# Kernel tuning notes

Measured on AMD Instinct MI355X. Metric: run time of the kernel, lower is better.

## Reference

```python
import jax, jax.numpy as jnp
import numpy as np

HEADS, DIM_HEAD, LANDMARKS, PINV_ITERS = 8, 64, 256, 6
DIM, SIZE, N_CLASSES, N_PATCH = 512, 1024, 2, 16384
LN_EPS = 1e-5


def layer_norm(x, g, b):
    mu = x.mean(-1, keepdims=True)
    var = ((x - mu) ** 2).mean(-1, keepdims=True)
    return (x - mu) / jnp.sqrt(var + LN_EPS) * g + b


def moore_penrose_pinv(x, iters):
    # x: [b, h, m, m]; global max over all batch/head entries (matches torch.max)
    abs_x = jnp.abs(x)
    col = abs_x.sum(-1).max()
    row = abs_x.sum(-2).max()
    z = jnp.swapaxes(x, -1, -2) / (col * row)
    I = jnp.eye(x.shape[-1], dtype=x.dtype)
    for _ in range(iters):
        xz = x @ z
        z = 0.25 * z @ (13 * I - xz @ (15 * I - xz @ (7 * I - xz)))
    return z


def nystrom_attention(x, qkv_w, out_w, out_b, res_w):
    b, n, _ = x.shape
    m = LANDMARKS
    pad = (m - n % m) % m
    xp = jnp.pad(x, ((0, 0), (pad, 0), (0, 0)))  # pad at FRONT of sequence
    npad = n + pad
    qkv = xp @ qkv_w  # [b, npad, 3*h*d]
    q, k, v = jnp.split(qkv, 3, axis=-1)
    to_h = lambda t: t.reshape(b, npad, HEADS, DIM_HEAD).transpose(0, 2, 1, 3)
    q, k, v = to_h(q), to_h(k), to_h(v)
    q = q * (DIM_HEAD ** -0.5)
    l = npad // m  # tokens per landmark segment
    q_l = q.reshape(b, HEADS, m, l, DIM_HEAD).sum(3) / l
    k_l = k.reshape(b, HEADS, m, l, DIM_HEAD).sum(3) / l
    sim1 = jnp.einsum('bhid,bhjd->bhij', q, k_l)     # [b,h,npad,m]
    sim2 = jnp.einsum('bhid,bhjd->bhij', q_l, k_l)   # [b,h,m,m]
    sim3 = jnp.einsum('bhid,bhjd->bhij', q_l, k)     # [b,h,m,npad]
    a1 = jax.nn.softmax(sim1, -1)
    a2 = jax.nn.softmax(sim2, -1)
    a3 = jax.nn.softmax(sim3, -1)
    out = (a1 @ moore_penrose_pinv(a2, PINV_ITERS)) @ (a3 @ v)
    # residual depthwise conv over sequence dim, kernel (33,1), groups=heads
    res = jax.lax.conv_general_dilated(
        v, res_w, (1, 1), [(16, 16), (0, 0)],
        dimension_numbers=('NCHW', 'OIHW', 'NCHW'), feature_group_count=HEADS)
    out = out + res
    out = out.transpose(0, 2, 1, 3).reshape(b, npad, HEADS * DIM_HEAD)
    out = out @ out_w + out_b
    return out[:, -n:]


def trans_layer(x, ng, nb, qkv_w, out_w, out_b, res_w):
    return x + nystrom_attention(layer_norm(x, ng, nb), qkv_w, out_w, out_b, res_w)


def ppeg(x, w7, b7, w5, b5, w3, b3, H, W):
    cls_tok, feat = x[:, :1], x[:, 1:]
    B, N, C = feat.shape
    f = feat.transpose(0, 2, 1).reshape(B, C, H, W)
    def dw(w, b, p):
        y = jax.lax.conv_general_dilated(
            f, w, (1, 1), [(p, p), (p, p)],
            dimension_numbers=('NCHW', 'OIHW', 'NCHW'), feature_group_count=C)
        return y + b[None, :, None, None]
    out = dw(w7, b7, 3) + f + dw(w5, b5, 2) + dw(w3, b3, 1)
    out = out.reshape(B, C, H * W).transpose(0, 2, 1)
    return jnp.concatenate([cls_tok, out], axis=1)


def setup_inputs() -> dict:
    key = jax.random.key(0)
    ks = jax.random.split(key, 24)
    rn = lambda k, s, sc=0.02: jax.random.normal(k, s, jnp.float32) * sc
    inner = HEADS * DIM_HEAD  # 512
    return {
        'data': jax.random.normal(ks[0], (1, N_PATCH, SIZE), jnp.float32),
        'fc1_w': rn(ks[1], (SIZE, DIM)), 'fc1_b': jnp.zeros((DIM,), jnp.float32),
        'cls_token': jax.random.normal(ks[2], (1, 1, DIM), jnp.float32),
        'l1_ng': jnp.ones((DIM,), jnp.float32), 'l1_nb': jnp.zeros((DIM,), jnp.float32),
        'l1_qkv': rn(ks[3], (DIM, 3 * inner)),
        'l1_ow': rn(ks[4], (inner, DIM)), 'l1_ob': jnp.zeros((DIM,), jnp.float32),
        'l1_rw': rn(ks[5], (HEADS, 1, 33, 1)),
        'l2_ng': jnp.ones((DIM,), jnp.float32), 'l2_nb': jnp.zeros((DIM,), jnp.float32),
        'l2_qkv': rn(ks[6], (DIM, 3 * inner)),
        'l2_ow': rn(ks[7], (inner, DIM)), 'l2_ob': jnp.zeros((DIM,), jnp.float32),
        'l2_rw': rn(ks[8], (HEADS, 1, 33, 1)),
        'p_w7': rn(ks[9], (DIM, 1, 7, 7)), 'p_b7': jnp.zeros((DIM,), jnp.float32),
        'p_w5': rn(ks[10], (DIM, 1, 5, 5)), 'p_b5': jnp.zeros((DIM,), jnp.float32),
        'p_w3': rn(ks[11], (DIM, 1, 3, 3)), 'p_b3': jnp.zeros((DIM,), jnp.float32),
        'n_g': jnp.ones((DIM,), jnp.float32), 'n_b': jnp.zeros((DIM,), jnp.float32),
        'fc2_w': rn(ks[12], (DIM, N_CLASSES)), 'fc2_b': jnp.zeros((N_CLASSES,), jnp.float32),
    }


def reference(data, fc1_w, fc1_b, cls_token, l1_ng, l1_nb, l1_qkv, l1_ow, l1_ob, l1_rw,
              l2_ng, l2_nb, l2_qkv, l2_ow, l2_ob, l2_rw,
              p_w7, p_b7, p_w5, p_b5, p_w3, p_b3, n_g, n_b, fc2_w, fc2_b):
    h = jax.nn.relu(data @ fc1_w + fc1_b)  # [B, N, 512]
    B, N = h.shape[0], h.shape[1]
    _H = _W = int(np.ceil(np.sqrt(N)))
    add_length = _H * _W - N
    h = jnp.concatenate([h, h[:, :add_length, :]], axis=1)
    cls = jnp.broadcast_to(cls_token, (B, 1, h.shape[2]))
    h = jnp.concatenate([cls, h], axis=1)
    h = trans_layer(h, l1_ng, l1_nb, l1_qkv, l1_ow, l1_ob, l1_rw)
    h = ppeg(h, p_w7, p_b7, p_w5, p_b5, p_w3, p_b3, _H, _W)
    h = trans_layer(h, l2_ng, l2_nb, l2_qkv, l2_ow, l2_ob, l2_rw)
    h = layer_norm(h, n_g, n_b)[:, 0]
    logits = h @ fc2_w + fc2_b
    y_hat = jnp.argmax(logits, axis=1)
    y_prob = jax.nn.softmax(logits, axis=1)
    return (logits, y_prob, y_hat)
```

## Files before the change

kernel.cpp:

```cpp
#include <hip/hip_runtime.h>
#include <hip/hip_bf16.h>


#define NT 16385
#define NP 16640
#define PADR 255
#define DIMF 512
#define QKVW 1536
#define NHEAD 8
#define DH 64
#define NLM 256
#define LSEG 65
#define A3V_TC 20

typedef short bf16x8 __attribute__((ext_vector_type(8)));
typedef short bf16x4 __attribute__((ext_vector_type(4)));
typedef float f32x4 __attribute__((ext_vector_type(4)));

__device__ __forceinline__ void gload_lds16(const void* g, void* l) {
    __builtin_amdgcn_global_load_lds(
        (const __attribute__((address_space(1))) void*)g,
        (__attribute__((address_space(3))) void*)l, 16, 0, 0);
}

__device__ __forceinline__ float2 b2f(const __hip_bfloat16* p) {
    ushort2 u = *(const ushort2*)p;
    float2 r;
    r.x = __uint_as_float((unsigned)u.x << 16);
    r.y = __uint_as_float((unsigned)u.y << 16);
    return r;
}

__device__ __forceinline__ unsigned f2b16(float a, float b) {
    union { unsigned u; __hip_bfloat16 h[2]; } c;
    c.h[0] = __float2bfloat16(a); c.h[1] = __float2bfloat16(b);
    return c.u;
}

__device__ __forceinline__ bf16x4 f4b(float a, float b, float c, float d) {
    union { bf16x4 v; __hip_bfloat16 h[4]; } u;
    u.h[0] = __float2bfloat16(a); u.h[1] = __float2bfloat16(b);
    u.h[2] = __float2bfloat16(c); u.h[3] = __float2bfloat16(d);
    return u.v;
}

__global__ __launch_bounds__(256) void gemm_bf16_k(
    const __hip_bfloat16* __restrict__ A, const __hip_bfloat16* __restrict__ BT,
    const float* __restrict__ bias, const float* __restrict__ Cacc,
    float* __restrict__ C, __hip_bfloat16* __restrict__ C16,
    int M, int N, int K, int MA, int relu)
{
    __shared__ __align__(16) __hip_bfloat16 Asl[2][128 * 64];
    __shared__ __align__(16) __hip_bfloat16 Bsl[2][128 * 64];
    int tid = threadIdx.x;
    int wid = tid >> 6, lane = tid & 63;
    int nwg = (int)(gridDim.x * gridDim.y);
    int orig = (int)(blockIdx.y * gridDim.x + blockIdx.x);
    int qq = nwg >> 3, rr = nwg & 7;
    int xcd = orig & 7, idx = orig >> 3;
    int wg = (xcd < rr ? xcd * (qq + 1) : rr * (qq + 1) + (xcd - rr) * qq) + idx;
    int m0 = (wg / (int)gridDim.x) << 7, n0 = (wg % (int)gridDim.x) << 7;
    int wr = (wid >> 1) << 6, wc = (wid & 1) << 6;
    f32x4 acc[4][4] = {};
    int lr = lane >> 3, lk = (lane & 7) << 3;
    int nt = K >> 6;
    auto stage = [&](int buf, int kt) {
#pragma unroll
        for (int i = 0; i < 4; ++i) {
            int ch = wid * 4 + i;
            int rowA = m0 + ch * 8 + lr;
            rowA = rowA < MA ? rowA : (MA - 1);
            gload_lds16(A + (size_t)rowA * K + kt + lk, &Asl[buf][ch * 512]);
            int rowB = n0 + ch * 8 + lr;
            gload_lds16(BT + (size_t)rowB * K + kt + lk, &Bsl[buf][ch * 512]);
        }
    };
    stage(0, 0);
    __syncthreads();
    int cur = 0;
    for (int t = 0; t < nt; ++t) {
        if (t + 1 < nt) stage(cur ^ 1, (t + 1) << 6);
#pragma unroll
        for (int ks = 0; ks < 2; ++ks) {
            int kb = ks * 32 + (lane >> 4) * 8;
            bf16x8 af[4], bfr[4];
#pragma unroll
            for (int m = 0; m < 4; ++m)
                af[m] = *(const bf16x8*)&Asl[cur][(wr + m * 16 + (lane & 15)) * 64 + kb];
#pragma unroll
            for (int n = 0; n < 4; ++n)
                bfr[n] = *(const bf16x8*)&Bsl[cur][(wc + n * 16 + (lane & 15)) * 64 + kb];
#pragma unroll
            for (int m = 0; m < 4; ++m)
#pragma unroll
                for (int n = 0; n < 4; ++n)
                    acc[m][n] = __builtin_amdgcn_mfma_f32_16x16x32_bf16(
                        af[m], bfr[n], acc[m][n], 0, 0, 0);
        }
        __syncthreads();
        cur ^= 1;
    }
    int cr = (lane >> 4) << 2, cc = lane & 15;
#pragma unroll
    for (int m = 0; m < 4; ++m) {
#pragma unroll
        for (int i = 0; i < 4; ++i) {
            int gm = m0 + wr + m * 16 + cr + i;
            if (gm >= M) continue;
#pragma unroll
            for (int n = 0; n < 4; ++n) {
                int gn = n0 + wc + n * 16 + cc;
                float v = acc[m][n][i];
                if (bias) v += bias[gn];
                if (Cacc) v += Cacc[(size_t)gm * N + gn];
                if (relu) v = fmaxf(v, 0.f);
                if (C16) C16[(size_t)gm * N + gn] = __float2bfloat16(v);
                else C[(size_t)gm * N + gn] = v;
            }
        }
    }
}

__global__ __launch_bounds__(256) void transcvt_k(const float* __restrict__ W,
    __hip_bfloat16* __restrict__ WT, int K, int N)
{
    __shared__ float t[32][33];
    int nt = N >> 5;
    int n0 = (blockIdx.x % nt) << 5, k0 = (blockIdx.x / nt) << 5;
    int tx = threadIdx.x & 31, ty = threadIdx.x >> 5;
    for (int r = ty; r < 32; r += 8) t[r][tx] = W[(size_t)(k0 + r) * N + n0 + tx];
    __syncthreads();
    for (int r = ty; r < 32; r += 8)
        WT[(size_t)(n0 + r) * K + k0 + tx] = __float2bfloat16(t[tx][r]);
}

__global__ __launch_bounds__(256) void cvt_k(const float4* __restrict__ in,
    ushort4* __restrict__ out, int n4)
{
    int i = blockIdx.x * 256 + threadIdx.x;
    if (i >= n4) return;
    float4 v = in[i];
    union { __hip_bfloat16 h[4]; ushort4 u; } cv;
    cv.h[0] = __float2bfloat16(v.x); cv.h[1] = __float2bfloat16(v.y);
    cv.h[2] = __float2bfloat16(v.z); cv.h[3] = __float2bfloat16(v.w);
    out[i] = cv.u;
}

__global__ __launch_bounds__(256) void vtrans_k(const __hip_bfloat16* __restrict__ qkvb16,
    __hip_bfloat16* __restrict__ vT16)
{
    int h = blockIdx.y;
    int t0 = blockIdx.x << 6;
    __shared__ float tile[64][65];
    int tid = threadIdx.x;
    for (int e = tid; e < 512; e += 256) {
        int r = e >> 3, c8 = (e & 7) << 3;
        union { bf16x8 v; __hip_bfloat16 hh[8]; } u;
        u.v = *(const bf16x8*)(qkvb16 + (size_t)(t0 + r) * QKVW + 1024 + (h << 6) + c8);
#pragma unroll
        for (int j = 0; j < 8; ++j) tile[r][c8 + j] = __bfloat162float(u.hh[j]);
    }
    __syncthreads();
    for (int e = tid; e < 512; e += 256) {
        int d = e >> 3, t8 = (e & 7) << 3;
        union { bf16x8 v; __hip_bfloat16 hh[8]; } u;
#pragma unroll
        for (int j = 0; j < 8; ++j) u.hh[j] = __float2bfloat16(tile[t8 + j][d]);
        *(bf16x8*)(vT16 + ((size_t)(h << 6) + d) * NP + t0 + t8) = u.v;
    }
}

__global__ __launch_bounds__(64) void ln_k(const float* __restrict__ in,
    const float* __restrict__ g, const float* __restrict__ b,
    __hip_bfloat16* __restrict__ out, int rows)
{
    int r = blockIdx.x;
    if (r >= rows) return;
    int lane = threadIdx.x;
    const float* xr = in + (size_t)r * DIMF;
    float v[8], s = 0.f;
#pragma unroll
    for (int i = 0; i < 8; ++i) { v[i] = xr[i * 64 + lane]; s += v[i]; }
#pragma unroll
    for (int off = 32; off; off >>= 1) s += __shfl_xor(s, off);
    float mu = s * (1.f / 512.f);
    float vs = 0.f;
#pragma unroll
    for (int i = 0; i < 8; ++i) { float d = v[i] - mu; vs += d * d; }
#pragma unroll
    for (int off = 32; off; off >>= 1) vs += __shfl_xor(vs, off);
    float rstd = rsqrtf(vs * (1.f / 512.f) + 1e-5f);
    __hip_bfloat16* orow = out + (size_t)r * DIMF;
#pragma unroll
    for (int i = 0; i < 8; ++i) {
        int d = i * 64 + lane;
        orow[d] = __float2bfloat16((v[i] - mu) * rstd * g[d] + b[d]);
    }
}

__global__ __launch_bounds__(256) void landmark_k(const __hip_bfloat16* __restrict__ qkvb16,
    float* __restrict__ ql, float* __restrict__ kl,
    __hip_bfloat16* __restrict__ ql16, __hip_bfloat16* __restrict__ kl16)
{
    int bx = blockIdx.x;
    int h = bx >> 8, j = bx & 255;
    int w = threadIdx.x >> 6, d = threadIdx.x & 63;
    __shared__ float pq[4][64], pk[4][64];
    float qs = 0.f, ks = 0.f;
    for (int u = w; u < LSEG; u += 4) {
        size_t addr = (size_t)(j * LSEG + u) * QKVW + (h << 6) + d;
        qs += __bfloat162float(qkvb16[addr]);
        ks += __bfloat162float(qkvb16[addr + 512]);
    }
    pq[w][d] = qs; pk[w][d] = ks;
    __syncthreads();
    if (threadIdx.x < 64) {
        float q = pq[0][d] + pq[1][d] + pq[2][d] + pq[3][d];
        float k = pk[0][d] + pk[1][d] + pk[2][d] + pk[3][d];
        float qm = q * (1.f / 65.f) * 0.125f;
        float km = k * (1.f / 65.f);
        ql[(size_t)bx * 64 + d] = qm;
        kl[(size_t)bx * 64 + d] = km;
        ql16[(size_t)bx * 64 + d] = __float2bfloat16(qm);
        kl16[(size_t)bx * 64 + d] = __float2bfloat16(km);
    }
}

__global__ __launch_bounds__(256) void a2_k(const float* __restrict__ ql,
    const float* __restrict__ kl, float* __restrict__ a2, __hip_bfloat16* __restrict__ a2_16)
{
    int h = blockIdx.x >> 8, i = blockIdx.x & 255;
    int j = threadIdx.x;
    __shared__ float qs[64];
    __shared__ float red[256];
    if (j < 64) qs[j] = ql[((size_t)(h << 8) + i) * 64 + j];
    __syncthreads();
    const float* kr = kl + ((size_t)(h << 8) + j) * 64;
    float s = 0.f;
#pragma unroll 8
    for (int d = 0; d < 64; ++d) s += qs[d] * kr[d];
    red[j] = s; __syncthreads();
    for (int st = 128; st; st >>= 1) { if (j < st) red[j] = fmaxf(red[j], red[j + st]); __syncthreads(); }
    float mx = red[0]; __syncthreads();
    float p = __expf(s - mx);
    red[j] = p; __syncthreads();
    for (int st = 128; st; st >>= 1) { if (j < st) red[j] += red[j + st]; __syncthreads(); }
    float v = p / red[0];
    a2[((size_t)h << 16) + i * 256 + j] = v;
    a2_16[((size_t)h << 16) + i * 256 + j] = __float2bfloat16(v);
}

__global__ __launch_bounds__(256) void zinit_k(const float* __restrict__ a2,
    __hip_bfloat16* __restrict__ zr16, __hip_bfloat16* __restrict__ zT16)
{
    int h = blockIdx.x, t = threadIdx.x;
    const float* X = a2 + ((size_t)h << 16);
    __shared__ float red[256];
    __shared__ float tl[64][65];
    float rs = 0.f;
    const float4* Xr = (const float4*)(X + (size_t)t * 256);
    for (int j = 0; j < 64; ++j) {
        float4 v = Xr[j];
        rs += fabsf(v.x) + fabsf(v.y) + fabsf(v.z) + fabsf(v.w);
    }
    red[t] = rs; __syncthreads();
    for (int st = 128; st; st >>= 1) { if (t < st) red[t] = fmaxf(red[t], red[t + st]); __syncthreads(); }
    float colv = red[0]; __syncthreads();
    float cs = 0.f;
    for (int i = 0; i < 256; ++i) cs += fabsf(X[i * 256 + t]);
    red[t] = cs; __syncthreads();
    for (int st = 128; st; st >>= 1) { if (t < st) red[t] = fmaxf(red[t], red[t + st]); __syncthreads(); }
    float rowv = red[0];
    float inv = 1.f / (colv * rowv);
    int cl = t & 63, rg = t >> 6;
    for (int tr = 0; tr < 4; ++tr)
        for (int tc = 0; tc < 4; ++tc) {
            __syncthreads();
#pragma unroll
            for (int k = 0; k < 16; ++k) {
                int rl = (k << 2) + rg;
                tl[rl][cl] = X[(size_t)(tr * 64 + rl) * 256 + tc * 64 + cl];
            }
            __syncthreads();
#pragma unroll
            for (int k = 0; k < 16; ++k) {
                int rl = (k << 2) + rg;
                zT16[((size_t)h << 16) + (size_t)(tr * 64 + rl) * 256 + tc * 64 + cl] =
                    __float2bfloat16(tl[rl][cl] * inv);
                zr16[((size_t)h << 16) + (size_t)(tc * 64 + rl) * 256 + tr * 64 + cl] =
                    __float2bfloat16(tl[cl][rl] * inv);
            }
        }
}

__global__ __launch_bounds__(256) void pgemm1_k(
    const __hip_bfloat16* __restrict__ a2_16, const __hip_bfloat16* __restrict__ zT16,
    __hip_bfloat16* __restrict__ xz16, __hip_bfloat16* __restrict__ t1T16)
{
    int h = blockIdx.y, n0 = blockIdx.x << 6;
    int lane = threadIdx.x & 63;
    int r0 = (threadIdx.x >> 6) << 6;
    int rA = lane & 15, g = lane >> 4, kp = g << 3;
    const __hip_bfloat16* Ah = a2_16 + ((size_t)h << 16);
    const __hip_bfloat16* Bh = zT16 + ((size_t)h << 16);
    f32x4 acc[4][4] = {};
    for (int ks = 0; ks < 8; ++ks) {
        bf16x8 af[4], bfr[4];
#pragma unroll
        for (int m = 0; m < 4; ++m)
            af[m] = *(const bf16x8*)&Ah[(size_t)(r0 + m * 16 + rA) * 256 + ks * 32 + kp];
#pragma unroll
        for (int n = 0; n < 4; ++n)
            bfr[n] = *(const bf16x8*)&Bh[(size_t)(n0 + n * 16 + rA) * 256 + ks * 32 + kp];
#pragma unroll
        for (int m = 0; m < 4; ++m)
#pragma unroll
            for (int n = 0; n < 4; ++n)
                acc[m][n] = __builtin_amdgcn_mfma_f32_16x16x32_bf16(af[m], bfr[n], acc[m][n], 0, 0, 0);
    }
    __hip_bfloat16* xzh = xz16 + ((size_t)h << 16);
    __hip_bfloat16* t1h = t1T16 + ((size_t)h << 16);
#pragma unroll
    for (int m = 0; m < 4; ++m)
#pragma unroll
        for (int i = 0; i < 4; ++i) {
            int gr = r0 + m * 16 + (g << 2) + i;
#pragma unroll
            for (int n = 0; n < 4; ++n) {
                int gc = n0 + n * 16 + rA;
                float v = acc[m][n][i];
                xzh[(size_t)gr * 256 + gc] = __float2bfloat16(v);
                t1h[(size_t)gc * 256 + gr] = __float2bfloat16((gr == gc ? 7.f : 0.f) - v);
            }
        }
}

__global__ __launch_bounds__(256) void pgemm3_k(
    const __hip_bfloat16* __restrict__ xz16, const __hip_bfloat16* __restrict__ t1T16,
    const __hip_bfloat16* __restrict__ zr16,
    __hip_bfloat16* __restrict__ znr16, __hip_bfloat16* __restrict__ znT16)
{
    __shared__ __align__(16) __hip_bfloat16 tA[64][264];
    __shared__ __align__(16) __hip_bfloat16 tB[64][264];
    int h = blockIdx.y, n0 = blockIdx.x << 6;
    int lane = threadIdx.x & 63;
    int r0 = (threadIdx.x >> 6) << 6;
    int rA = lane & 15, g = lane >> 4, kp = g << 3;
    const __hip_bfloat16* Xh = xz16 + ((size_t)h << 16);
    const __hip_bfloat16* T1h = t1T16 + ((size_t)h << 16);
    {
        f32x4 acc[4][4] = {};
        for (int ks = 0; ks < 8; ++ks) {
            bf16x8 af[4], bfr[4];
#pragma unroll
            for (int m = 0; m < 4; ++m)
                af[m] = *(const bf16x8*)&Xh[(size_t)(r0 + m * 16 + rA) * 256 + ks * 32 + kp];
#pragma unroll
            for (int n = 0; n < 4; ++n)
                bfr[n] = *(const bf16x8*)&T1h[(size_t)(n0 + n * 16 + rA) * 256 + ks * 32 + kp];
#pragma unroll
            for (int m = 0; m < 4; ++m)
#pragma unroll
                for (int n = 0; n < 4; ++n)
                    acc[m][n] = __builtin_amdgcn_mfma_f32_16x16x32_bf16(af[m], bfr[n], acc[m][n], 0, 0, 0);
        }
#pragma unroll
        for (int m = 0; m < 4; ++m)
#pragma unroll
            for (int n = 0; n < 4; ++n) {
                int gr0 = r0 + m * 16 + (g << 2);
                int cl = n * 16 + rA;
                *(bf16x4*)&tA[cl][gr0] = f4b(
                    ((gr0 + 0 == n0 + cl) ? 15.f : 0.f) - acc[m][n][0],
                    ((gr0 + 1 == n0 + cl) ? 15.f : 0.f) - acc[m][n][1],
                    ((gr0 + 2 == n0 + cl) ? 15.f : 0.f) - acc[m][n][2],
                    ((gr0 + 3 == n0 + cl) ? 15.f : 0.f) - acc[m][n][3]);
            }
    }
    __syncthreads();
    {
        f32x4 acc[4][4] = {};
        for (int ks = 0; ks < 8; ++ks) {
            bf16x8 af[4], bfr[4];
#pragma unroll
            for (int m = 0; m < 4; ++m)
                af[m] = *(const bf16x8*)&Xh[(size_t)(r0 + m * 16 + rA) * 256 + ks * 32 + kp];
#pragma unroll
            for (int n = 0; n < 4; ++n)
                bfr[n] = *(const bf16x8*)&tA[n * 16 + rA][ks * 32 + kp];
#pragma unroll
            for (int m = 0; m < 4; ++m)
#pragma unroll
                for (int n = 0; n < 4; ++n)
                    acc[m][n] = __builtin_amdgcn_mfma_f32_16x16x32_bf16(af[m], bfr[n], acc[m][n], 0, 0, 0);
        }
#pragma unroll
        for (int m = 0; m < 4; ++m)
#pragma unroll
            for (int n = 0; n < 4; ++n) {
                int gr0 = r0 + m * 16 + (g << 2);
                int cl = n * 16 + rA;
                *(bf16x4*)&tB[cl][gr0] = f4b(
                    ((gr0 + 0 == n0 + cl) ? 13.f : 0.f) - acc[m][n][0],
                    ((gr0 + 1 == n0 + cl) ? 13.f : 0.f) - acc[m][n][1],
                    ((gr0 + 2 == n0 + cl) ? 13.f : 0.f) - acc[m][n][2],
                    ((gr0 + 3 == n0 + cl) ? 13.f : 0.f) - acc[m][n][3]);
            }
    }
    __syncthreads();
    {
        const __hip_bfloat16* Zh = zr16 + ((size_t)h << 16);
        f32x4 acc[4][4] = {};
        for (int ks = 0; ks < 8; ++ks) {
            bf16x8 af[4], bfr[4];
#pragma unroll
            for (int m = 0; m < 4; ++m)
                af[m] = *(const bf16x8*)&Zh[(size_t)(r0 + m * 16 + rA) * 256 + ks * 32 + kp];
#pragma unroll
            for (int n = 0; n < 4; ++n)
                bfr[n] = *(const bf16x8*)&tB[n * 16 + rA][ks * 32 + kp];
#pragma unroll
            for (int m = 0; m < 4; ++m)
#pragma unroll
                for (int n = 0; n < 4; ++n)
                    acc[m][n] = __builtin_amdgcn_mfma_f32_16x16x32_bf16(af[m], bfr[n], acc[m][n], 0, 0, 0);
        }
        __hip_bfloat16* zrh = znr16 + ((size_t)h << 16);
        __hip_bfloat16* zth = znT16 + ((size_t)h << 16);
#pragma unroll
        for (int m = 0; m < 4; ++m)
#pragma unroll
            for (int i = 0; i < 4; ++i) {
                int gr = r0 + m * 16 + (g << 2) + i;
#pragma unroll
                for (int n = 0; n < 4; ++n) {
                    int gc = n0 + n * 16 + rA;
                    float v = 0.25f * acc[m][n][i];
                    zrh[(size_t)gr * 256 + gc] = __float2bfloat16(v);
                    zth[(size_t)gc * 256 + gr] = __float2bfloat16(v);
                }
            }
    }
}

__global__ __launch_bounds__(256) void wm_k(
    const __hip_bfloat16* __restrict__ zr16, const __hip_bfloat16* __restrict__ a3vT16,
    __hip_bfloat16* __restrict__ wmT16)
{
    int h = blockIdx.x;
    int lane = threadIdx.x & 63;
    int r0 = (threadIdx.x >> 6) << 6;
    int rA = lane & 15, g = lane >> 4, kp = g << 3;
    const __hip_bfloat16* Zh = zr16 + ((size_t)h << 16);
    const __hip_bfloat16* Bh = a3vT16 + ((size_t)h << 14);
    f32x4 acc[4][4] = {};
    for (int ks = 0; ks < 8; ++ks) {
        bf16x8 af[4], bfr[4];
#pragma unroll
        for (int m = 0; m < 4; ++m)
            af[m] = *(const bf16x8*)&Zh[(size_t)(r0 + m * 16 + rA) * 256 + ks * 32 + kp];
#pragma unroll
        for (int n = 0; n < 4; ++n)
            bfr[n] = *(const bf16x8*)&Bh[(size_t)(n * 16 + rA) * 256 + ks * 32 + kp];
#pragma unroll
        for (int m = 0; m < 4; ++m)
#pragma unroll
            for (int n = 0; n < 4; ++n)
                acc[m][n] = __builtin_amdgcn_mfma_f32_16x16x32_bf16(af[m], bfr[n], acc[m][n], 0, 0, 0);
    }
    __hip_bfloat16* Wh = wmT16 + ((size_t)h << 14);
#pragma unroll
    for (int m = 0; m < 4; ++m)
#pragma unroll
        for (int i = 0; i < 4; ++i) {
            int gr = r0 + m * 16 + (g << 2) + i;
#pragma unroll
            for (int n = 0; n < 4; ++n)
                Wh[(size_t)(n * 16 + rA) * 256 + gr] = __float2bfloat16(acc[m][n][i]);
        }
}

__global__ __launch_bounds__(128) void a3v_flash_k(
    const __hip_bfloat16* __restrict__ ql16, const __hip_bfloat16* __restrict__ qkvb16,
    const __hip_bfloat16* __restrict__ vT16,
    float* __restrict__ opart, float* __restrict__ mpart, float* __restrict__ lpart)
{
    int bx = blockIdx.x;
    int h = bx >> 2, qb = bx & 3;
    int tc = blockIdx.y;
    int wv = threadIdx.x >> 6;
    int lane = threadIdx.x & 63;
    int rA = lane & 15, g = lane >> 4, kp = g << 3;
    __shared__ __align__(16) __hip_bfloat16 Plds[2][32 * 64];
    char* P = (char*)&Plds[wv][0];

    bf16x8 qa[2][2];
    const __hip_bfloat16* qlh = ql16 + ((size_t)h << 14);
#pragma unroll
    for (int m = 0; m < 2; ++m)
#pragma unroll
        for (int ks = 0; ks < 2; ++ks)
            qa[m][ks] = *(const bf16x8*)(qlh +
                (size_t)((qb << 6) + (wv << 5) + (m << 4) + rA) * 64 + ks * 32 + kp);

    const __hip_bfloat16* kg = qkvb16 + 512 + (h << 6);
    const __hip_bfloat16* vg = vT16 + ((size_t)(h << 6)) * NP;

    f32x4 O[2][4] = {};
    float m_[2][4], l_[2][4];
#pragma unroll
    for (int m = 0; m < 2; ++m)
#pragma unroll
        for (int i = 0; i < 4; ++i) { m_[m][i] = -3e38f; l_[m][i] = 0.f; }

    for (int tile = tc * 13; tile < tc * 13 + 13; ++tile) {
        int t0 = tile << 6;
        f32x4 S[2][4] = {};
#pragma unroll
        for (int n = 0; n < 4; ++n)
#pragma unroll
            for (int ks = 0; ks < 2; ++ks) {
                bf16x8 kb = *(const bf16x8*)(kg + (size_t)(t0 + (n << 4) + rA) * QKVW + ks * 32 + kp);
                S[0][n] = __builtin_amdgcn_mfma_f32_16x16x32_bf16(qa[0][ks], kb, S[0][n], 0, 0, 0);
                S[1][n] = __builtin_amdgcn_mfma_f32_16x16x32_bf16(qa[1][ks], kb, S[1][n], 0, 0, 0);
            }
        float f_[2][4];
#pragma unroll
        for (int m = 0; m < 2; ++m)
#pragma unroll
            for (int i = 0; i < 4; ++i) {
                float mx = fmaxf(fmaxf(S[m][0][i], S[m][1][i]), fmaxf(S[m][2][i], S[m][3][i]));
#pragma unroll
                for (int msk = 8; msk; msk >>= 1) mx = fmaxf(mx, __shfl_xor(mx, msk));
                float mn = fmaxf(m_[m][i], mx);
                float f = __expf(m_[m][i] - mn);
                int r = (m << 4) + (g << 2) + i;
                int swz = (r & 7) << 4;
                float sum = 0.f;
#pragma unroll
                for (int n = 0; n < 4; ++n) {
                    float p = __expf(S[m][n][i] - mn);
                    sum += p;
                    int byte = (r << 7) + (((n << 4) + rA) << 1);
                    *(__hip_bfloat16*)(P + (byte ^ swz)) = __float2bfloat16(p);
                }
#pragma unroll
                for (int msk = 8; msk; msk >>= 1) sum += __shfl_xor(sum, msk);
                l_[m][i] = l_[m][i] * f + sum;
                m_[m][i] = mn;
                f_[m][i] = f;
            }
#pragma unroll
        for (int m = 0; m < 2; ++m)
#pragma unroll
            for (int i = 0; i < 4; ++i) {
                float f = f_[m][i];
#pragma unroll
                for (int n = 0; n < 4; ++n) O[m][n][i] *= f;
            }
#pragma unroll
        for (int ks2 = 0; ks2 < 2; ++ks2) {
            bf16x8 pa[2];
#pragma unroll
            for (int m = 0; m < 2; ++m) {
                int rr = (m << 4) + rA;
                int byte = (rr << 7) + ((ks2 * 32 + kp) << 1);
                pa[m] = *(const bf16x8*)(P + (byte ^ ((rr & 7) << 4)));
            }
#pragma unroll
            for (int n = 0; n < 4; ++n) {
                bf16x8 vb = *(const bf16x8*)(vg + (size_t)((n << 4) + rA) * NP + t0 + ks2 * 32 + kp);
                O[0][n] = __builtin_amdgcn_mfma_f32_16x16x32_bf16(pa[0], vb, O[0][n], 0, 0, 0);
                O[1][n] = __builtin_amdgcn_mfma_f32_16x16x32_bf16(pa[1], vb, O[1][n], 0, 0, 0);
            }
        }
    }
    int pb2 = (bx << 1) | wv;
    size_t obase = ((size_t)pb2 * A3V_TC + tc) * 2048;
#pragma unroll
    for (int m = 0; m < 2; ++m)
#pragma unroll
        for (int i = 0; i < 4; ++i) {
            int r = (m << 4) + (g << 2) + i;
#pragma unroll
            for (int n = 0; n < 4; ++n)
                opart[obase + (size_t)r * 64 + (n << 4) + rA] = O[m][n][i];
            if (rA == 0) {
                mpart[((size_t)pb2 * A3V_TC + tc) * 32 + r] = m_[m][i];
                lpart[((size_t)pb2 * A3V_TC + tc) * 32 + r] = l_[m][i];
            }
        }
}

__global__ __launch_bounds__(64) void a3v_comb_k(const float* __restrict__ opart,
// ... 172 lines not shown
    for (int e = tid; e < 196 * 16; e += 256) {
        int sp = e >> 4, cp = (e & 15) << 1;
        int yy = ty0 - 3 + sp / 14, xc = tx0 - 3 + sp % 14;
        float2 v = make_float2(0.f, 0.f);
        if ((unsigned)yy < 128u && (unsigned)xc < 128u)
            v = *(const float2*)&feat[(size_t)(yy * 128 + xc) * DIMF + (cg << 5) + cp];
        *(unsigned*)&tile[sp][cp] = f2b16(v.x, v.y);
    }
    __syncthreads();
    float2 bs7 = *(const float2*)&b7[c], bs5 = *(const float2*)&b5[c], bs3 = *(const float2*)&b3[c];
    float bsx = bs7.x + bs5.x + bs3.x, bsy = bs7.y + bs5.y + bs3.y;
    float2 acc[4];
#pragma unroll
    for (int o = 0; o < 4; ++o) {
        float2 idv = *(const float2*)&feat[(size_t)((ty0 + yb0 + o) * 128 + tx0 + xo) * DIMF + c];
        acc[o].x = idv.x + bsx;
        acc[o].y = idv.y + bsy;
    }
    int c2 = cgi << 1;
#pragma unroll
    for (int kx = 0; kx < 7; ++kx) {
        float2 wc[7];
#pragma unroll
        for (int j = 0; j < 7; ++j) wc[j] = b2f(&ws7[j * 7 + kx][c2]);
#pragma unroll
        for (int r = 0; r < 10; ++r) {
            float2 v = b2f(&tile[(yb0 + r) * 14 + xo + kx][c2]);
#pragma unroll
            for (int o = 0; o < 4; ++o) {
                int ky = r - o;
                if (ky >= 0 && ky < 7) {
                    acc[o].x += wc[ky].x * v.x; acc[o].y += wc[ky].y * v.y;
                }
            }
        }
    }
#pragma unroll
    for (int kx = 0; kx < 5; ++kx) {
        float2 wc[5];
#pragma unroll
        for (int j = 0; j < 5; ++j) wc[j] = b2f(&ws5[j * 5 + kx][c2]);
#pragma unroll
        for (int r = 0; r < 8; ++r) {
            float2 v = b2f(&tile[(yb0 + 1 + r) * 14 + xo + 1 + kx][c2]);
#pragma unroll
            for (int o = 0; o < 4; ++o) {
                int ky = r - o;
                if (ky >= 0 && ky < 5) {
                    acc[o].x += wc[ky].x * v.x; acc[o].y += wc[ky].y * v.y;
                }
            }
        }
    }
#pragma unroll
    for (int kx = 0; kx < 3; ++kx) {
        float2 wc[3];
#pragma unroll
        for (int j = 0; j < 3; ++j) wc[j] = b2f(&ws3[j * 3 + kx][c2]);
#pragma unroll
        for (int r = 0; r < 6; ++r) {
            float2 v = b2f(&tile[(yb0 + 2 + r) * 14 + xo + 2 + kx][c2]);
#pragma unroll
            for (int o = 0; o < 4; ++o) {
                int ky = r - o;
                if (ky >= 0 && ky < 3) {
                    acc[o].x += wc[ky].x * v.x; acc[o].y += wc[ky].y * v.y;
                }
            }
        }
    }
#pragma unroll
    for (int o = 0; o < 4; ++o)
        *(float2*)&outfeat[(size_t)((ty0 + yb0 + o) * 128 + tx0 + xo) * DIMF + c] = acc[o];
}

__global__ __launch_bounds__(64) void head_k(const float* __restrict__ x,
    const float* __restrict__ g, const float* __restrict__ b,
    const float* __restrict__ w, const float* __restrict__ bias, float* __restrict__ out)
{
    int lane = threadIdx.x;
    float v[8], s = 0.f;
#pragma unroll
    for (int i = 0; i < 8; ++i) { v[i] = x[i * 64 + lane]; s += v[i]; }
#pragma unroll
    for (int off = 32; off; off >>= 1) s += __shfl_xor(s, off);
    float mu = s * (1.f / 512.f);
    float vs = 0.f;
#pragma unroll
    for (int i = 0; i < 8; ++i) { float d = v[i] - mu; vs += d * d; }
#pragma unroll
    for (int off = 32; off; off >>= 1) vs += __shfl_xor(vs, off);
    float rstd = rsqrtf(vs * (1.f / 512.f) + 1e-5f);
    float l0 = 0.f, l1 = 0.f;
#pragma unroll
    for (int i = 0; i < 8; ++i) {
        int d = i * 64 + lane;
        float hn = (v[i] - mu) * rstd * g[d] + b[d];
        l0 += hn * w[d * 2];
        l1 += hn * w[d * 2 + 1];
    }
#pragma unroll
    for (int off = 32; off; off >>= 1) { l0 += __shfl_xor(l0, off); l1 += __shfl_xor(l1, off); }
    if (lane == 0) {
        l0 += bias[0]; l1 += bias[1];
        float m = fmaxf(l0, l1);
        float e0 = __expf(l0 - m), e1 = __expf(l1 - m);
        float ss = e0 + e1;
        out[0] = l0; out[1] = l1;
        out[2] = e0 / ss; out[3] = e1 / ss;
        out[4] = (l1 > l0) ? 1.f : 0.f;
    }
}

extern "C" void kernel_launch(void* const* d_in, const int* in_sizes, int n_in,
                              void* d_out, int out_size, void* d_ws, size_t ws_size,
                              hipStream_t stream)
{
    (void)in_sizes; (void)n_in; (void)out_size; (void)ws_size;
    const float* data   = (const float*)d_in[0];
    const float* fc1_w  = (const float*)d_in[1];
    const float* fc1_b  = (const float*)d_in[2];
    const float* cls    = (const float*)d_in[3];
    const float* l1_ng  = (const float*)d_in[4];
    const float* l1_nb  = (const float*)d_in[5];
    const float* l1_qkv = (const float*)d_in[6];
    const float* l1_ow  = (const float*)d_in[7];
    const float* l1_ob  = (const float*)d_in[8];
    const float* l1_rw  = (const float*)d_in[9];
    const float* l2_ng  = (const float*)d_in[10];
    const float* l2_nb  = (const float*)d_in[11];
    const float* l2_qkv = (const float*)d_in[12];
    const float* l2_ow  = (const float*)d_in[13];
    const float* l2_ob  = (const float*)d_in[14];
    const float* l2_rw  = (const float*)d_in[15];
    const float* p_w7   = (const float*)d_in[16];
    const float* p_b7   = (const float*)d_in[17];
    const float* p_w5   = (const float*)d_in[18];
    const float* p_b5   = (const float*)d_in[19];
    const float* p_w3   = (const float*)d_in[20];
    const float* p_b3   = (const float*)d_in[21];
    const float* n_g    = (const float*)d_in[22];
    const float* n_b    = (const float*)d_in[23];
    const float* fc2_w  = (const float*)d_in[24];
    const float* fc2_b  = (const float*)d_in[25];

    char* base = (char*)d_ws;
    auto carve = [&](size_t bytes) { char* p = base; base += (bytes + 255) & ~(size_t)255; return p; };
    float* x               = (float*)carve((size_t)NT * DIMF * 4);
    float* x2              = (float*)carve((size_t)NT * DIMF * 4);
    __hip_bfloat16* xp16   = (__hip_bfloat16*)carve((size_t)NP * DIMF * 2);
    __hip_bfloat16* qkvb16 = (__hip_bfloat16*)carve((size_t)NP * QKVW * 2);
    __hip_bfloat16* vT16   = (__hip_bfloat16*)carve((size_t)NHEAD * DH * NP * 2);
    __hip_bfloat16* obuf16 = (__hip_bfloat16*)carve((size_t)NP * DIMF * 2);
    float* obuf            = (float*)carve((size_t)NP * DIMF * 4);
    __hip_bfloat16* wT     = (__hip_bfloat16*)carve((size_t)QKVW * DIMF * 2);
    float* ql              = (float*)carve(131072 * 4);
    float* kl              = (float*)carve(131072 * 4);
    __hip_bfloat16* ql16   = (__hip_bfloat16*)carve(131072 * 2);
    __hip_bfloat16* kl16   = (__hip_bfloat16*)carve(131072 * 2);
    __hip_bfloat16* wmT16  = (__hip_bfloat16*)carve(131072 * 2);
    float* a2              = (float*)carve(524288 * 4);
    __hip_bfloat16* a2_16  = (__hip_bfloat16*)carve(524288 * 2);
    __hip_bfloat16* zrA    = (__hip_bfloat16*)carve(524288 * 2);
    __hip_bfloat16* zrB    = (__hip_bfloat16*)carve(524288 * 2);
    __hip_bfloat16* ztA    = (__hip_bfloat16*)carve(524288 * 2);
    __hip_bfloat16* ztB    = (__hip_bfloat16*)carve(524288 * 2);
    __hip_bfloat16* xz16   = (__hip_bfloat16*)carve(524288 * 2);
    __hip_bfloat16* t1T16  = (__hip_bfloat16*)carve(524288 * 2);
    __hip_bfloat16* a3vT16 = (__hip_bfloat16*)carve(131072 * 2);
    float* opart = (float*)carve((size_t)64 * A3V_TC * 2048 * 4);
    float* mpart = (float*)carve((size_t)64 * A3V_TC * 32 * 4);
    float* lpart = (float*)carve((size_t)64 * A3V_TC * 32 * 4);
    __hip_bfloat16* obuf2  = xp16;
    __hip_bfloat16* data16 = qkvb16;

    cvt_k<<<(16384 * 1024 / 4 + 255) / 256, 256, 0, stream>>>(
        (const float4*)data, (ushort4*)data16, 16384 * 1024 / 4);
    transcvt_k<<<(DIMF / 32) * (1024 / 32), 256, 0, stream>>>(fc1_w, wT, 1024, DIMF);
    gemm_bf16_k<<<dim3(DIMF / 128, 16384 / 128), 256, 0, stream>>>(
        data16, wT, fc1_b, nullptr, x + DIMF, nullptr, 16384, DIMF, 1024, 16384, 1);
    hipMemcpyAsync(x, cls, DIMF * sizeof(float), hipMemcpyDeviceToDevice, stream);

    auto layer = [&](float* xv, const float* ng, const float* nb, const float* qw,
                     const float* ow, const float* ob, const float* rw) {
        hipMemsetAsync(xp16, 0, (size_t)PADR * DIMF * 2, stream);
        ln_k<<<NT, 64, 0, stream>>>(xv, ng, nb, xp16 + (size_t)PADR * DIMF, NT);
        transcvt_k<<<(QKVW / 32) * (DIMF / 32), 256, 0, stream>>>(qw, wT, DIMF, QKVW);
        gemm_bf16_k<<<dim3(QKVW / 128, NP / 128), 256, 0, stream>>>(
            xp16, wT, nullptr, nullptr, nullptr, qkvb16, NP, QKVW, DIMF, NP, 0);
        vtrans_k<<<dim3(NP / 64, NHEAD), 256, 0, stream>>>(qkvb16, vT16);
        landmark_k<<<NHEAD * NLM, 256, 0, stream>>>(qkvb16, ql, kl, ql16, kl16);
        a2_k<<<NHEAD * NLM, 256, 0, stream>>>(ql, kl, a2, a2_16);
        zinit_k<<<NHEAD, 256, 0, stream>>>(a2, zrA, ztA);
        __hip_bfloat16 *zr = zrA, *zt = ztA, *zrN = zrB, *ztN = ztB;
        for (int it = 0; it < 6; ++it) {
            pgemm1_k<<<dim3(4, NHEAD), 256, 0, stream>>>(a2_16, zt, xz16, t1T16);
            pgemm3_k<<<dim3(4, NHEAD), 256, 0, stream>>>(xz16, t1T16, zr, zrN, ztN);
            __hip_bfloat16* t;
            t = zr; zr = zrN; zrN = t;
            t = zt; zt = ztN; ztN = t;
        }
        a3v_flash_k<<<dim3(32, A3V_TC), 128, 0, stream>>>(ql16, qkvb16, vT16, opart, mpart, lpart);
        a3v_comb_k<<<64, 64, 0, stream>>>(opart, mpart, lpart, a3vT16);
        wm_k<<<NHEAD, 256, 0, stream>>>(zr, a3vT16, wmT16);
        attnout_mfma_k<<<dim3(NP / 64, NHEAD), 128, 0, stream>>>(qkvb16, kl16, wmT16, obuf16);
        resconv_tile_k<<<dim3(NP / 128, NHEAD), 256, 0, stream>>>(qkvb16, rw, obuf16, obuf2);
        transcvt_k<<<(DIMF / 32) * (DIMF / 32), 256, 0, stream>>>(ow, wT, DIMF, DIMF);
        gemm_bf16_k<<<dim3(DIMF / 128, (NT + 127) / 128), 256, 0, stream>>>(
            obuf2 + (size_t)PADR * DIMF, wT, ob, xv, xv, nullptr, NT, DIMF, DIMF, NT, 0);
    };

    layer(x, l1_ng, l1_nb, l1_qkv, l1_ow, l1_ob, l1_rw);

    ppeg3_k<<<dim3(256, 16), 256, 0, stream>>>(x, p_w7, p_b7, p_w5, p_b5, p_w3, p_b3, x2 + DIMF);
    hipMemcpyAsync(x2, x, DIMF * sizeof(float), hipMemcpyDeviceToDevice, stream);

    layer(x2, l2_ng, l2_nb, l2_qkv, l2_ow, l2_ob, l2_rw);

    head_k<<<1, 64, 0, stream>>>(x2, n_g, n_b, fc2_w, fc2_b, (float*)d_out);
}
```

Measured before the change: 1.410 ms.

## Fuse pinv iterations into one cooperative kernel and drop GEMM double buffering

Replaces the twelve per-iteration pgemm1/pgemm3 launches of the Newton-Schulz pseudo-inverse with a single cooperative kernel of 32 blocks that uses grid-wide syncs between phases. This is meant to remove kernel launch overhead and inter-kernel gaps in the small 256x256 iteration. Separately, the main bf16 GEMM loses its double-buffered LDS staging and now loads and computes each K tile in turn, which halves LDS use but serialises global loads with MFMA work. An unused fp32 output buffer allocation is also removed. With an even iteration count the final z lands back in zrA, so wm_k reads zrA.

```diff
diff --git a/kernel.cpp b/kernel.cpp
--- a/kernel.cpp
+++ b/kernel.cpp
@@ -1,5 +1,8 @@
 #include <hip/hip_runtime.h>
 #include <hip/hip_bf16.h>
+#include <hip/hip_cooperative_groups.h>
+
+namespace cg = cooperative_groups;
 
 
 #define NT 16385
@@ -50,8 +53,8 @@
     float* __restrict__ C, __hip_bfloat16* __restrict__ C16,
     int M, int N, int K, int MA, int relu)
 {
-    __shared__ __align__(16) __hip_bfloat16 Asl[2][128 * 64];
-    __shared__ __align__(16) __hip_bfloat16 Bsl[2][128 * 64];
+    __shared__ __align__(16) __hip_bfloat16 Asl[128 * 64];
+    __shared__ __align__(16) __hip_bfloat16 Bsl[128 * 64];
     int tid = threadIdx.x;
     int wid = tid >> 6, lane = tid & 63;
     int nwg = (int)(gridDim.x * gridDim.y);
@@ -63,33 +66,27 @@
     int wr = (wid >> 1) << 6, wc = (wid & 1) << 6;
     f32x4 acc[4][4] = {};
     int lr = lane >> 3, lk = (lane & 7) << 3;
-    int nt = K >> 6;
-    auto stage = [&](int buf, int kt) {
+    for (int kt = 0; kt < K; kt += 64) {
 #pragma unroll
         for (int i = 0; i < 4; ++i) {
             int ch = wid * 4 + i;
             int rowA = m0 + ch * 8 + lr;
             rowA = rowA < MA ? rowA : (MA - 1);
-            gload_lds16(A + (size_t)rowA * K + kt + lk, &Asl[buf][ch * 512]);
+            gload_lds16(A + (size_t)rowA * K + kt + lk, &Asl[ch * 512]);
             int rowB = n0 + ch * 8 + lr;
-            gload_lds16(BT + (size_t)rowB * K + kt + lk, &Bsl[buf][ch * 512]);
-        }
-    };
-    stage(0, 0);
-    __syncthreads();
-    int cur = 0;
-    for (int t = 0; t < nt; ++t) {
-        if (t + 1 < nt) stage(cur ^ 1, (t + 1) << 6);
+            gload_lds16(BT + (size_t)rowB * K + kt + lk, &Bsl[ch * 512]);
+        }
+        __syncthreads();
 #pragma unroll
         for (int ks = 0; ks < 2; ++ks) {
             int kb = ks * 32 + (lane >> 4) * 8;
             bf16x8 af[4], bfr[4];
 #pragma unroll
             for (int m = 0; m < 4; ++m)
-                af[m] = *(const bf16x8*)&Asl[cur][(wr + m * 16 + (lane & 15)) * 64 + kb];
+                af[m] = *(const bf16x8*)&Asl[(wr + m * 16 + (lane & 15)) * 64 + kb];
 #pragma unroll
             for (int n = 0; n < 4; ++n)
-                bfr[n] = *(const bf16x8*)&Bsl[cur][(wc + n * 16 + (lane & 15)) * 64 + kb];
+                bfr[n] = *(const bf16x8*)&Bsl[(wc + n * 16 + (lane & 15)) * 64 + kb];
 #pragma unroll
             for (int m = 0; m < 4; ++m)
 #pragma unroll
@@ -98,7 +95,6 @@
                         af[m], bfr[n], acc[m][n], 0, 0, 0);
         }
         __syncthreads();
-        cur ^= 1;
     }
     int cr = (lane >> 4) << 2, cc = lane & 15;
 #pragma unroll
@@ -293,153 +289,155 @@
         }
 }
 
-__global__ __launch_bounds__(256) void pgemm1_k(
-    const __hip_bfloat16* __restrict__ a2_16, const __hip_bfloat16* __restrict__ zT16,
+__global__ __launch_bounds__(256) void pinv_coop_k(
+    const __hip_bfloat16* __restrict__ a2_16,
+    __hip_bfloat16* zr0, __hip_bfloat16* zr1,
+    __hip_bfloat16* zt0, __hip_bfloat16* zt1,
     __hip_bfloat16* __restrict__ xz16, __hip_bfloat16* __restrict__ t1T16)
 {
-    int h = blockIdx.y, n0 = blockIdx.x << 6;
+    __shared__ __align__(16) __hip_bfloat16 tA[64][264];
+    __shared__ __align__(16) __hip_bfloat16 tB[64][264];
+    cg::grid_group gg = cg::this_grid();
+    int bid = (int)blockIdx.x;
+    int h = bid >> 2, n0 = (bid & 3) << 6;
     int lane = threadIdx.x & 63;
     int r0 = (threadIdx.x >> 6) << 6;
     int rA = lane & 15, g = lane >> 4, kp = g << 3;
     const __hip_bfloat16* Ah = a2_16 + ((size_t)h << 16);
-    const __hip_bfloat16* Bh = zT16 + ((size_t)h << 16);
-    f32x4 acc[4][4] = {};
-    for (int ks = 0; ks < 8; ++ks) {
-        bf16x8 af[4], bfr[4];
-#pragma unroll
-        for (int m = 0; m < 4; ++m)
-            af[m] = *(const bf16x8*)&Ah[(size_t)(r0 + m * 16 + rA) * 256 + ks * 32 + kp];
-#pragma unroll
-        for (int n = 0; n < 4; ++n)
-            bfr[n] = *(const bf16x8*)&Bh[(size_t)(n0 + n * 16 + rA) * 256 + ks * 32 + kp];
-#pragma unroll
-        for (int m = 0; m < 4; ++m)
-#pragma unroll
-            for (int n = 0; n < 4; ++n)
-                acc[m][n] = __builtin_amdgcn_mfma_f32_16x16x32_bf16(af[m], bfr[n], acc[m][n], 0, 0, 0);
-    }
     __hip_bfloat16* xzh = xz16 + ((size_t)h << 16);
     __hip_bfloat16* t1h = t1T16 + ((size_t)h << 16);
-#pragma unroll
-    for (int m = 0; m < 4; ++m)
-#pragma unroll
-        for (int i = 0; i < 4; ++i) {
-            int gr = r0 + m * 16 + (g << 2) + i;
-#pragma unroll
-            for (int n = 0; n < 4; ++n) {
-                int gc = n0 + n * 16 + rA;
-                float v = acc[m][n][i];
-                xzh[(size_t)gr * 256 + gc] = __float2bfloat16(v);
-                t1h[(size_t)gc * 256 + gr] = __float2bfloat16((gr == gc ? 7.f : 0.f) - v);
-            }
-        }
-}
-
-__global__ __launch_bounds__(256) void pgemm3_k(
-    const __hip_bfloat16* __restrict__ xz16, const __hip_bfloat16* __restrict__ t1T16,
-    const __hip_bfloat16* __restrict__ zr16,
-    __hip_bfloat16* __restrict__ znr16, __hip_bfloat16* __restrict__ znT16)
-{
-    __shared__ __align__(16) __hip_bfloat16 tA[64][264];
-    __shared__ __align__(16) __hip_bfloat16 tB[64][264];
-    int h = blockIdx.y, n0 = blockIdx.x << 6;
-    int lane = threadIdx.x & 63;
-    int r0 = (threadIdx.x >> 6) << 6;
-    int rA = lane & 15, g = lane >> 4, kp = g << 3;
-    const __hip_bfloat16* Xh = xz16 + ((size_t)h << 16);
-    const __hip_bfloat16* T1h = t1T16 + ((size_t)h << 16);
-    {
-        f32x4 acc[4][4] = {};
-        for (int ks = 0; ks < 8; ++ks) {
-            bf16x8 af[4], bfr[4];
+    __hip_bfloat16* zr = zr0; __hip_bfloat16* zt = zt0;
+    __hip_bfloat16* zrN = zr1; __hip_bfloat16* ztN = zt1;
+    for (int it = 0; it < 6; ++it) {
+        {
+            const __hip_bfloat16* Bh = zt + ((size_t)h << 16);
+            f32x4 acc[4][4] = {};
+            for (int ks = 0; ks < 8; ++ks) {
+                bf16x8 af[4], bfr[4];
+#pragma unroll
+                for (int m = 0; m < 4; ++m)
+                    af[m] = *(const bf16x8*)&Ah[(size_t)(r0 + m * 16 + rA) * 256 + ks * 32 + kp];
+#pragma unroll
+                for (int n = 0; n < 4; ++n)
+                    bfr[n] = *(const bf16x8*)&Bh[(size_t)(n0 + n * 16 + rA) * 256 + ks * 32 + kp];
+#pragma unroll
+                for (int m = 0; m < 4; ++m)
+#pragma unroll
+                    for (int n = 0; n < 4; ++n)
+                        acc[m][n] = __builtin_amdgcn_mfma_f32_16x16x32_bf16(af[m], bfr[n], acc[m][n], 0, 0, 0);
+            }
 #pragma unroll
             for (int m = 0; m < 4; ++m)
-                af[m] = *(const bf16x8*)&Xh[(size_t)(r0 + m * 16 + rA) * 256 + ks * 32 + kp];
-#pragma unroll
-            for (int n = 0; n < 4; ++n)
-                bfr[n] = *(const bf16x8*)&T1h[(size_t)(n0 + n * 16 + rA) * 256 + ks * 32 + kp];
+#pragma unroll
+                for (int i = 0; i < 4; ++i) {
+                    int gr = r0 + m * 16 + (g << 2) + i;
+#pragma unroll
+                    for (int n = 0; n < 4; ++n) {
+                        int gc = n0 + n * 16 + rA;
+                        float v = acc[m][n][i];
+                        xzh[(size_t)gr * 256 + gc] = __float2bfloat16(v);
+                        t1h[(size_t)gc * 256 + gr] = __float2bfloat16((gr == gc ? 7.f : 0.f) - v);
+                    }
+                }
+        }
+        gg.sync();
+        {
+            f32x4 acc[4][4] = {};
+            for (int ks = 0; ks < 8; ++ks) {
+                bf16x8 af[4], bfr[4];
+#pragma unroll
+                for (int m = 0; m < 4; ++m)
+                    af[m] = *(const bf16x8*)&xzh[(size_t)(r0 + m * 16 + rA) * 256 + ks * 32 + kp];
+#pragma unroll
+                for (int n = 0; n < 4; ++n)
+                    bfr[n] = *(const bf16x8*)&t1h[(size_t)(n0 + n * 16 + rA) * 256 + ks * 32 + kp];
+#pragma unroll
+                for (int m = 0; m < 4; ++m)
+#pragma unroll
+                    for (int n = 0; n < 4; ++n)
+                        acc[m][n] = __builtin_amdgcn_mfma_f32_16x16x32_bf16(af[m], bfr[n], acc[m][n], 0, 0, 0);
+            }
 #pragma unroll
             for (int m = 0; m < 4; ++m)
 #pragma unroll
+                for (int n = 0; n < 4; ++n) {
+                    int gr0 = r0 + m * 16 + (g << 2);
+                    int cl = n * 16 + rA;
+                    *(bf16x4*)&tA[cl][gr0] = f4b(
+                        ((gr0 + 0 == n0 + cl) ? 15.f : 0.f) - acc[m][n][0],
+                        ((gr0 + 1 == n0 + cl) ? 15.f : 0.f) - acc[m][n][1],
+                        ((gr0 + 2 == n0 + cl) ? 15.f : 0.f) - acc[m][n][2],
+                        ((gr0 + 3 == n0 + cl) ? 15.f : 0.f) - acc[m][n][3]);
+                }
+        }
+        __syncthreads();
+        {
+            f32x4 acc[4][4] = {};
+            for (int ks = 0; ks < 8; ++ks) {
+                bf16x8 af[4], bfr[4];
+#pragma unroll
+                for (int m = 0; m < 4; ++m)
+                    af[m] = *(const bf16x8*)&xzh[(size_t)(r0 + m * 16 + rA) * 256 + ks * 32 + kp];
+#pragma unroll
                 for (int n = 0; n < 4; ++n)
-                    acc[m][n] = __builtin_amdgcn_mfma_f32_16x16x32_bf16(af[m], bfr[n], acc[m][n], 0, 0, 0);
-        }
-#pragma unroll
-        for (int m = 0; m < 4; ++m)
-#pragma unroll
-            for (int n = 0; n < 4; ++n) {
-                int gr0 = r0 + m * 16 + (g << 2);
-                int cl = n * 16 + rA;
-                *(bf16x4*)&tA[cl][gr0] = f4b(
-                    ((gr0 + 0 == n0 + cl) ? 15.f : 0.f) - acc[m][n][0],
-                    ((gr0 + 1 == n0 + cl) ? 15.f : 0.f) - acc[m][n][1],
-                    ((gr0 + 2 == n0 + cl) ? 15.f : 0.f) - acc[m][n][2],
-                    ((gr0 + 3 == n0 + cl) ? 15.f : 0.f) - acc[m][n][3]);
-            }
-    }
-    __syncthreads();
-    {
-        f32x4 acc[4][4] = {};
-        for (int ks = 0; ks < 8; ++ks) {
-            bf16x8 af[4], bfr[4];
+                    bfr[n] = *(const bf16x8*)&tA[n * 16 + rA][ks * 32 + kp];
+#pragma unroll
+                for (int m = 0; m < 4; ++m)
+#pragma unroll
+                    for (int n = 0; n < 4; ++n)
+                        acc[m][n] = __builtin_amdgcn_mfma_f32_16x16x32_bf16(af[m], bfr[n], acc[m][n], 0, 0, 0);
+            }
 #pragma unroll
             for (int m = 0; m < 4; ++m)
-                af[m] = *(const bf16x8*)&Xh[(size_t)(r0 + m * 16 + rA) * 256 + ks * 32 + kp];
-#pragma unroll
-            for (int n = 0; n < 4; ++n)
-                bfr[n] = *(const bf16x8*)&tA[n * 16 + rA][ks * 32 + kp];
+#pragma unroll
+                for (int n = 0; n < 4; ++n) {
+                    int gr0 = r0 + m * 16 + (g << 2);
+                    int cl = n * 16 + rA;
+                    *(bf16x4*)&tB[cl][gr0] = f4b(
+                        ((gr0 + 0 == n0 + cl) ? 13.f : 0.f) - acc[m][n][0],
+                        ((gr0 + 1 == n0 + cl) ? 13.f : 0.f) - acc[m][n][1],
+                        ((gr0 + 2 == n0 + cl) ? 13.f : 0.f) - acc[m][n][2],
+                        ((gr0 + 3 == n0 + cl) ? 13.f : 0.f) - acc[m][n][3]);
+                }
+        }
+        __syncthreads();
+        {
+            const __hip_bfloat16* Zh = zr + ((size_t)h << 16);
+            f32x4 acc[4][4] = {};
+            for (int ks = 0; ks < 8; ++ks) {
+                bf16x8 af[4], bfr[4];
+#pragma unroll
+                for (int m = 0; m < 4; ++m)
+                    af[m] = *(const bf16x8*)&Zh[(size_t)(r0 + m * 16 + rA) * 256 + ks * 32 + kp];
+#pragma unroll
+                for (int n = 0; n < 4; ++n)
+                    bfr[n] = *(const bf16x8*)&tB[n * 16 + rA][ks * 32 + kp];
+#pragma unroll
+                for (int m = 0; m < 4; ++m)
+#pragma unroll
+                    for (int n = 0; n < 4; ++n)
+                        acc[m][n] = __builtin_amdgcn_mfma_f32_16x16x32_bf16(af[m], bfr[n], acc[m][n], 0, 0, 0);
+            }
+            __hip_bfloat16* zrh = zrN + ((size_t)h << 16);
+            __hip_bfloat16* zth = ztN + ((size_t)h << 16);
 #pragma unroll
             for (int m = 0; m < 4; ++m)
 #pragma unroll
-                for (int n = 0; n < 4; ++n)
-                    acc[m][n] = __builtin_amdgcn_mfma_f32_16x16x32_bf16(af[m], bfr[n], acc[m][n], 0, 0, 0);
-        }
-#pragma unroll
-        for (int m = 0; m < 4; ++m)
-#pragma unroll
-            for (int n = 0; n < 4; ++n) {
-                int gr0 = r0 + m * 16 + (g << 2);
-                int cl = n * 16 + rA;
-                *(bf16x4*)&tB[cl][gr0] = f4b(
-                    ((gr0 + 0 == n0 + cl) ? 13.f : 0.f) - acc[m][n][0],
-                    ((gr0 + 1 == n0 + cl) ? 13.f : 0.f) - acc[m][n][1],
-                    ((gr0 + 2 == n0 + cl) ? 13.f : 0.f) - acc[m][n][2],
-                    ((gr0 + 3 == n0 + cl) ? 13.f : 0.f) - acc[m][n][3]);
-            }
-    }
-    __syncthreads();
-    {
-        const __hip_bfloat16* Zh = zr16 + ((size_t)h << 16);
-        f32x4 acc[4][4] = {};
-        for (int ks = 0; ks < 8; ++ks) {
-            bf16x8 af[4], bfr[4];
-#pragma unroll
-            for (int m = 0; m < 4; ++m)
-                af[m] = *(const bf16x8*)&Zh[(size_t)(r0 + m * 16 + rA) * 256 + ks * 32 + kp];
-#pragma unroll
-            for (int n = 0; n < 4; ++n)
-                bfr[n] = *(const bf16x8*)&tB[n * 16 + rA][ks * 32 + kp];
-#pragma unroll
-            for (int m = 0; m < 4; ++m)
-#pragma unroll
-                for (int n = 0; n < 4; ++n)
-                    acc[m][n] = __builtin_amdgcn_mfma_f32_16x16x32_bf16(af[m], bfr[n], acc[m][n], 0, 0, 0);
-        }
-        __hip_bfloat16* zrh = znr16 + ((size_t)h << 16);
-        __hip_bfloat16* zth = znT16 + ((size_t)h << 16);
-#pragma unroll
-        for (int m = 0; m < 4; ++m)
-#pragma unroll
-            for (int i = 0; i < 4; ++i) {
-                int gr = r0 + m * 16 + (g << 2) + i;
-#pragma unroll
-                for (int n = 0; n < 4; ++n) {
-                    int gc = n0 + n * 16 + rA;
-                    float v = 0.25f * acc[m][n][i];
-                    zrh[(size_t)gr * 256 + gc] = __float2bfloat16(v);
-                    zth[(size_t)gc * 256 + gr] = __float2bfloat16(v);
+                for (int i = 0; i < 4; ++i) {
+                    int gr = r0 + m * 16 + (g << 2) + i;
+#pragma unroll
+                    for (int n = 0; n < 4; ++n) {
+                        int gc = n0 + n * 16 + rA;
+                        float v = 0.25f * acc[m][n][i];
+                        zrh[(size_t)gr * 256 + gc] = __float2bfloat16(v);
+                        zth[(size_t)gc * 256 + gr] = __float2bfloat16(v);
+                    }
                 }
-            }
+        }
+        gg.sync();
+        __hip_bfloat16* t;
+        t = zr; zr = zrN; zrN = t;
+        t = zt; zt = ztN; ztN = t;
     }
 }
 
@@ -918,7 +916,6 @@
     __hip_bfloat16* qkvb16 = (__hip_bfloat16*)carve((size_t)NP * QKVW * 2);
     __hip_bfloat16* vT16   = (__hip_bfloat16*)carve((size_t)NHEAD * DH * NP * 2);
     __hip_bfloat16* obuf16 = (__hip_bfloat16*)carve((size_t)NP * DIMF * 2);
-    float* obuf            = (float*)carve((size_t)NP * DIMF * 4);
     __hip_bfloat16* wT     = (__hip_bfloat16*)carve((size_t)QKVW * DIMF * 2);
     float* ql              = (float*)carve(131072 * 4);
     float* kl              = (float*)carve(131072 * 4);
@@ -958,17 +955,17 @@
         landmark_k<<<NHEAD * NLM, 256, 0, stream>>>(qkvb16, ql, kl, ql16, kl16);
         a2_k<<<NHEAD * NLM, 256, 0, stream>>>(ql, kl, a2, a2_16);
         zinit_k<<<NHEAD, 256, 0, stream>>>(a2, zrA, ztA);
-        __hip_bfloat16 *zr = zrA, *zt = ztA, *zrN = zrB, *ztN = ztB;
-        for (int it = 0; it < 6; ++it) {
-            pgemm1_k<<<dim3(4, NHEAD), 256, 0, stream>>>(a2_16, zt, xz16, t1T16);
-            pgemm3_k<<<dim3(4, NHEAD), 256, 0, stream>>>(xz16, t1T16, zr, zrN, ztN);
-            __hip_bfloat16* t;
-            t = zr; zr = zrN; zrN = t;
-            t = zt; zt = ztN; ztN = t;
+        {
+            const __hip_bfloat16* a2c = a2_16;
+            __hip_bfloat16 *p0 = zrA, *p1 = zrB, *p2 = ztA, *p3 = ztB, *p4 = xz16, *p5 = t1T16;
+            void* kargs[] = { (void*)&a2c, (void*)&p0, (void*)&p1, (void*)&p2,
+                              (void*)&p3, (void*)&p4, (void*)&p5 };
+            hipLaunchCooperativeKernel((const void*)pinv_coop_k, dim3(32), dim3(256),
+                                       kargs, 0, stream);
         }
         a3v_flash_k<<<dim3(32, A3V_TC), 128, 0, stream>>>(ql16, qkvb16, vT16, opart, mpart, lpart);
         a3v_comb_k<<<64, 64, 0, stream>>>(opart, mpart, lpart, a3vT16);
-        wm_k<<<NHEAD, 256, 0, stream>>>(zr, a3vT16, wmT16);
+        wm_k<<<NHEAD, 256, 0, stream>>>(zrA, a3vT16, wmT16);
         attnout_mfma_k<<<dim3(NP / 64, NHEAD), 128, 0, stream>>>(qkvb16, kl16, wmT16, obuf16);
         resconv_tile_k<<<dim3(NP / 128, NHEAD), 256, 0, stream>>>(qkvb16, rw, obuf16, obuf2);
         transcvt_k<<<(DIMF / 32) * (DIMF / 32), 256, 0, stream>>>(ow, wT, DIMF, DIMF);
```

Result: slower. 1.573 ms (+11.6%).
